# Kernel tuning notes

Hardware: AMD Instinct MI355X
Metric: run time of the kernel (lower is better)

## Reference

```python
import jax, jax.numpy as jnp
import numpy as np

N_NODES = 100000
N_EDGES = 3200000
F_IN = 256
N_CLASSES = 10


def setup_inputs() -> dict:
    key = jax.random.key(0)
    ks = jax.random.split(key, 10)
    x = jax.random.normal(ks[0], (N_NODES, F_IN), dtype=jnp.float32)
    edge_index = jax.random.randint(ks[1], (2, N_EDGES), 0, N_NODES, dtype=jnp.int64)
    def glorot(k, fan_in, fan_out):
        s = (6.0 / (fan_in + fan_out)) ** 0.5
        return jax.random.uniform(k, (fan_in, fan_out), jnp.float32, -s, s)
    return {
        "x": x,
        "edge_index": edge_index,
        "W_gcn": glorot(ks[2], F_IN, 64),
        "b_gcn": jnp.zeros((64,), jnp.float32),
        "W1": glorot(ks[3], 64, 32),
        "b1": jnp.zeros((32,), jnp.float32),
        "W2": glorot(ks[4], 32, 16),
        "b2": jnp.zeros((16,), jnp.float32),
        "W3": glorot(ks[5], 16, N_CLASSES),
        "b3": jnp.zeros((N_CLASSES,), jnp.float32),
    }


def gcn_conv(x, edge_index, W, b):
    # PyG GCNConv: x' = D^{-1/2} (A + I) D^{-1/2} (x W) + b, with self-loops.
    n = x.shape[0]
    loop = jnp.arange(n, dtype=edge_index.dtype)
    src = jnp.concatenate([edge_index[0], loop])  # [E+N]
    dst = jnp.concatenate([edge_index[1], loop])
    deg = jax.ops.segment_sum(jnp.ones(src.shape, jnp.float32), dst, num_segments=n)
    dinv = jnp.where(deg > 0, jax.lax.rsqrt(deg), 0.0)
    norm = dinv[src] * dinv[dst]  # [E+N]
    h = x @ W  # transform first (reduces message width to 64)
    msg = h[src] * norm[:, None]  # gather + scale
    out = jax.ops.segment_sum(msg, dst, num_segments=n)  # scatter-add
    return out + b


def reference(x, edge_index, W_gcn, b_gcn, W1, b1, W2, b2, W3, b3):
    # Dropout is a no-op in eval mode; reference uses deterministic eval math.
    h = jax.nn.relu(gcn_conv(x, edge_index, W_gcn, b_gcn))
    h = jax.nn.relu(h @ W1 + b1)
    h = jax.nn.relu(h @ W2 + b2)
    return h @ W3 + b3
```

## Files before the change

### kernel.cpp

```cpp
#include <hip/hip_runtime.h>

#define F_IN 256
#define CHUNK 8192

typedef short bf8_t __attribute__((ext_vector_type(8)));
typedef float f4_t  __attribute__((ext_vector_type(4)));

__device__ __forceinline__ unsigned short f2bf(float f) {
  unsigned u = __float_as_uint(f);
  unsigned r = (u + 0x7FFFu + ((u >> 16) & 1u)) >> 16;
  return (unsigned short)r;
}
#define BF_LO(d) __uint_as_float((d) << 16)
#define BF_HI(d) __uint_as_float((d) & 0xFFFF0000u)

__global__ __launch_bounds__(256) void gemm_mfma_kernel(
    const float* __restrict__ x, const float* __restrict__ W,
    const float* __restrict__ dinvp, unsigned short* __restrict__ hb, int M) {
  __shared__ short As[128][40];
  __shared__ short Bs[64][264];
  const int t = threadIdx.x;
  const int brow = blockIdx.x * 128;
  const int w = t >> 6;
  const int l = t & 63;
  const int mlane = l & 15;
  const int quad = l >> 4;

  for (int i = 0; i < 64; ++i) {
    const int flat = i * 256 + t;
    const int k = flat >> 6, n = flat & 63;
    Bs[n][k] = (short)f2bf(W[flat]);
  }

  f4_t acc[2][4];
#pragma unroll
  for (int a = 0; a < 2; ++a)
#pragma unroll
    for (int b = 0; b < 4; ++b) acc[a][b] = (f4_t){0.f, 0.f, 0.f, 0.f};

  for (int k0 = 0; k0 < F_IN; k0 += 32) {
    {
      const int q = t & 7;
      const int rbase = t >> 3;
#pragma unroll
      for (int j = 0; j < 4; ++j) {
        const int r = rbase + j * 32;
        const int row = brow + r;
        float4 v = make_float4(0.f, 0.f, 0.f, 0.f);
        if (row < M) v = *(const float4*)(x + (size_t)row * F_IN + k0 + (q << 2));
        short* p = &As[r][q << 2];
        p[0] = (short)f2bf(v.x);
        p[1] = (short)f2bf(v.y);
        p[2] = (short)f2bf(v.z);
        p[3] = (short)f2bf(v.w);
      }
    }
    __syncthreads();
    bf8_t afr[2], bfr[4];
#pragma unroll
    for (int mt = 0; mt < 2; ++mt)
      afr[mt] = *(const bf8_t*)&As[w * 32 + mt * 16 + mlane][quad << 3];
#pragma unroll
    for (int nt = 0; nt < 4; ++nt)
      bfr[nt] = *(const bf8_t*)&Bs[nt * 16 + mlane][k0 + (quad << 3)];
#pragma unroll
    for (int mt = 0; mt < 2; ++mt)
#pragma unroll
      for (int nt = 0; nt < 4; ++nt)
        acc[mt][nt] = __builtin_amdgcn_mfma_f32_16x16x32_bf16(
            afr[mt], bfr[nt], acc[mt][nt], 0, 0, 0);
    __syncthreads();
  }

#pragma unroll
  for (int mt = 0; mt < 2; ++mt) {
#pragma unroll
    for (int reg = 0; reg < 4; ++reg) {
      const int row = brow + w * 32 + mt * 16 + (quad << 2) + reg;
      if (row < M) {
        const float di = dinvp[row];
#pragma unroll
        for (int nt = 0; nt < 4; ++nt)
          hb[(size_t)row * 64 + nt * 16 + mlane] = f2bf(di * acc[mt][nt][reg]);
      }
    }
  }
}

__global__ __launch_bounds__(512) void sort_local_kernel(
    const int* __restrict__ src_arr, const int* __restrict__ dst_arr,
    int* __restrict__ espB, int* __restrict__ segStart, int* __restrict__ segCnt,
    int* __restrict__ bucketCount, int E, int NBK) {
  __shared__ int hist[512];
  __shared__ int s[512];
  __shared__ int cur[512];
  const int t = threadIdx.x;
  const int blk = blockIdx.x;
  const int base = blk * CHUNK;
  const int cnt = min(CHUNK, E - base);
  for (int i = t; i < NBK; i += 512) hist[i] = 0;
  __syncthreads();
  int pk[16], bk[16];
#pragma unroll
  for (int k = 0; k < 16; ++k) {
    const int i = t + k * 512;
    bk[k] = -1;
    if (i < cnt) {
      const int sv = src_arr[base + i];
      const int dv = dst_arr[base + i];
      pk[k] = sv | ((dv & 255) << 24);
      bk[k] = dv >> 8;
      atomicAdd(&hist[bk[k]], 1);
    }
  }
  __syncthreads();
  const int v = (t < NBK) ? hist[t] : 0;
  s[t] = v;
  __syncthreads();
#pragma unroll
  for (int off = 1; off < 512; off <<= 1) {
    int add = (t >= off) ? s[t - off] : 0;
    __syncthreads();
    s[t] += add;
    __syncthreads();
  }
  if (t < NBK) {
    const int excl = s[t] - v;
    cur[t] = excl;
    segStart[blk * NBK + t] = base + excl;
    segCnt[blk * NBK + t] = v;
    if (v) atomicAdd(&bucketCount[t], v);
  }
  __syncthreads();
#pragma unroll
  for (int k = 0; k < 16; ++k) {
    if (bk[k] >= 0) {
      const int pos = atomicAdd(&cur[bk[k]], 1);
      espB[base + pos] = pk[k];
    }
  }
}

__global__ __launch_bounds__(512) void scan_buckets_kernel(
    const int* __restrict__ bucketCount, int* __restrict__ bucketStart, int NBK) {
  __shared__ int s[512];
  const int t = threadIdx.x;
  const int v = (t < NBK) ? bucketCount[t] : 0;
  s[t] = v;
  __syncthreads();
#pragma unroll
  for (int off = 1; off < 512; off <<= 1) {
    int add = (t >= off) ? s[t - off] : 0;
    __syncthreads();
    s[t] += add;
    __syncthreads();
  }
  if (t < NBK) bucketStart[t] = s[t] - v;
  if (t == NBK - 1) bucketStart[NBK] = s[t];
}

__global__ __launch_bounds__(512) void fine_bin2_kernel(
    const int* __restrict__ espB, const int* __restrict__ segStart,
    const int* __restrict__ segCnt, const int* __restrict__ bucketStart,
    int* __restrict__ es, int* __restrict__ rowptr, float* __restrict__ dinvp,
    int N, int E, int NBK, int NCH) {
  __shared__ int segS[512];
  __shared__ int segC[512];
  __shared__ int sbuf[512];
  __shared__ int hist[256];
  __shared__ int cur[256];
  const int t = threadIdx.x;
  const int b = blockIdx.x;
  for (int i = t; i < 512; i += 512) { segS[i] = 0; segC[i] = 0; }
  if (t < 256) hist[t] = 0;
  __syncthreads();
  for (int i = t; i < NCH; i += 512) {
    segS[i] = segStart[i * NBK + b];
    segC[i] = segCnt[i * NBK + b];
  }
  __syncthreads();

  const int wid = t >> 6;
  const int lane = t & 63;

  for (int seg = wid; seg < NCH; seg += 8) {
    const int sS = segS[seg], c = segC[seg];
    for (int j = lane; j < c; j += 64)
      atomicAdd(&hist[((unsigned)espB[sS + j]) >> 24], 1);
  }
  __syncthreads();

  int v2 = 0;
  if (t < 256) { v2 = hist[t]; sbuf[t] = v2; }
  __syncthreads();
#pragma unroll
  for (int off = 1; off < 256; off <<= 1) {
    int add = 0;
    if (t < 256 && t >= off) add = sbuf[t - off];
    __syncthreads();
    if (t < 256) sbuf[t] += add;
    __syncthreads();
  }
  const int base = bucketStart[b];
  if (t < 256) {
    const int excl = sbuf[t] - v2;
    cur[t] = base + excl;
    const int node = b * 256 + t;
    if (node < N) {
      rowptr[node] = base + excl;
      dinvp[node] = rsqrtf((float)(v2 + 1));
    }
  }
  if (b == 0 && t == 0) rowptr[N] = E;
  __syncthreads();

  for (int seg = wid; seg < NCH; seg += 8) {
    const int sS = segS[seg], c = segC[seg];
    for (int j = lane; j < c; j += 64) {
      const int p = espB[sS + j];
      const int pos = atomicAdd(&cur[((unsigned)p) >> 24], 1);
      es[pos] = p & 0x00FFFFFF;
    }
  }
}

__global__ __launch_bounds__(256) void agg_csr_kernel(
    const unsigned short* __restrict__ hb, const int* __restrict__ es,
    const int* __restrict__ rowptr, const float* __restrict__ dinvp,
    float* __restrict__ agg, int N) {
  const int t = threadIdx.x;
  const int node = blockIdx.x * 4 + (t >> 6);
  if (node >= N) return;
  const int lane = t & 63;
  const int slot = lane >> 3;
  const int fq = (lane & 7) << 3;
  const int start = rowptr[node];
  const int end = rowptr[node + 1];

  float acc[8] = {0.f};
  int i = start + slot;
  for (; i + 8 < end; i += 16) {
    const int s0 = es[i];
    const int s1 = es[i + 8];
    const uint4 r0 = *(const uint4*)(hb + (size_t)s0 * 64 + fq);
    const uint4 r1 = *(const uint4*)(hb + (size_t)s1 * 64 + fq);
    acc[0] += BF_LO(r0.x) + BF_LO(r1.x);
    acc[1] += BF_HI(r0.x) + BF_HI(r1.x);
    acc[2] += BF_LO(r0.y) + BF_LO(r1.y);
    acc[3] += BF_HI(r0.y) + BF_HI(r1.y);
    acc[4] += BF_LO(r0.z) + BF_LO(r1.z);
    acc[5] += BF_HI(r0.z) + BF_HI(r1.z);
    acc[6] += BF_LO(r0.w) + BF_LO(r1.w);
    acc[7] += BF_HI(r0.w) + BF_HI(r1.w);
  }
  if (i < end) {
    const int s0 = es[i];
    const uint4 r0 = *(const uint4*)(hb + (size_t)s0 * 64 + fq);
    acc[0] += BF_LO(r0.x);
    acc[1] += BF_HI(r0.x);
    acc[2] += BF_LO(r0.y);
    acc[3] += BF_HI(r0.y);
    acc[4] += BF_LO(r0.z);
    acc[5] += BF_HI(r0.z);
    acc[6] += BF_LO(r0.w);
    acc[7] += BF_HI(r0.w);
  }
#pragma unroll
  for (int m = 8; m <= 32; m <<= 1)
#pragma unroll
    for (int j = 0; j < 8; ++j) acc[j] += __shfl_xor(acc[j], m, 64);

  if (slot == 0) {
    const float di = dinvp[node];
    float4 o0 = make_float4(acc[0] * di, acc[1] * di, acc[2] * di, acc[3] * di);
    float4 o1 = make_float4(acc[4] * di, acc[5] * di, acc[6] * di, acc[7] * di);
    float* ap = agg + (size_t)node * 64 + fq;
    *(float4*)(ap + 0) = o0;
    *(float4*)(ap + 4) = o1;
  }
}

__global__ __launch_bounds__(256) void mlp_mfma_kernel(
    const float* __restrict__ agg, const unsigned short* __restrict__ hb,
    const float* __restrict__ dinvp, const float* __restrict__ bg,
    const float* __restrict__ W1, const float* __restrict__ b1,
    const float* __restrict__ W2, const float* __restrict__ b2,
    const float* __restrict__ W3, const float* __restrict__ b3,
    float* __restrict__ out, int N) {
  __shared__ short g64[256 * 72];
  __shared__ short h2s[256 * 40];
  __shared__ short W1s[32 * 72];
  __shared__ short W2s[16 * 40];
  __shared__ short W3s[16 * 40];
  __shared__ float bgs[64], b1s[32], b2s[16], b3s[16];
  short* h1s = g64;

  const int t = threadIdx.x;
  const int node0 = blockIdx.x * 256;
  for (int i = t; i < 256 * 40; i += 256) h2s[i] = 0;
  for (int i = t; i < 16 * 40; i += 256) W3s[i] = 0;
  if (t < 64) bgs[t] = bg[t];
  if (t < 32) b1s[t] = b1[t];
  if (t < 16) { b2s[t] = b2[t]; b3s[t] = (t < 10) ? b3[t] : 0.f; }
  __syncthreads();
  for (int i = t; i < 2048; i += 256) { const int k = i >> 5, n = i & 31; W1s[n * 72 + k] = (short)f2bf(W1[i]); }
  for (int i = t; i < 512;  i += 256) { const int k = i >> 4, n = i & 15; W2s[n * 40 + k] = (short)f2bf(W2[i]); }
  if (t < 160) { const int k = t / 10, n = t % 10; W3s[n * 40 + k] = (short)f2bf(W3[t]); }
  {
    const int nd = min(node0 + t, N - 1);
    const float di = dinvp[nd];
    short* gr = &g64[t * 72];
    const float* ar = agg + (size_t)nd * 64;
    const unsigned short* hr = hb + (size_t)nd * 64;
#pragma unroll
    for (int k = 0; k < 64; k += 8) {
      const float4 a0 = *(const float4*)(ar + k);
      const float4 a1 = *(const float4*)(ar + k + 4);
      const uint4 r = *(const uint4*)(hr + k);
      gr[k + 0] = (short)f2bf(fmaxf(a0.x + di * BF_LO(r.x) + bgs[k + 0], 0.f));
      gr[k + 1] = (short)f2bf(fmaxf(a0.y + di * BF_HI(r.x) + bgs[k + 1], 0.f));
      gr[k + 2] = (short)f2bf(fmaxf(a0.z + di * BF_LO(r.y) + bgs[k + 2], 0.f));
      gr[k + 3] = (short)f2bf(fmaxf(a0.w + di * BF_HI(r.y) + bgs[k + 3], 0.f));
      gr[k + 4] = (short)f2bf(fmaxf(a1.x + di * BF_LO(r.z) + bgs[k + 4], 0.f));
      gr[k + 5] = (short)f2bf(fmaxf(a1.y + di * BF_HI(r.z) + bgs[k + 5], 0.f));
      gr[k + 6] = (short)f2bf(fmaxf(a1.z + di * BF_LO(r.w) + bgs[k + 6], 0.f));
      gr[k + 7] = (short)f2bf(fmaxf(a1.w + di * BF_HI(r.w) + bgs[k + 7], 0.f));
    }
  }
  __syncthreads();

  const int w = t >> 6;
  const int lane = t & 63;
  const int ml = lane & 15;
  const int quad = lane >> 4;

  bf8_t a1f[4][2], b1f[2][2];
#pragma unroll
  for (int mt = 0; mt < 4; ++mt)
#pragma unroll
    for (int ks = 0; ks < 2; ++ks)
      a1f[mt][ks] = *(const bf8_t*)&g64[(w * 64 + mt * 16 + ml) * 72 + ks * 32 + quad * 8];
#pragma unroll
  for (int nt = 0; nt < 2; ++nt)
#pragma unroll
    for (int ks = 0; ks < 2; ++ks)
      b1f[nt][ks] = *(const bf8_t*)&W1s[(nt * 16 + ml) * 72 + ks * 32 + quad * 8];
  f4_t acc1[4][2];
#pragma unroll
  for (int mt = 0; mt < 4; ++mt)
#pragma unroll
    for (int nt = 0; nt < 2; ++nt) acc1[mt][nt] = (f4_t){0.f, 0.f, 0.f, 0.f};
#pragma unroll
  for (int ks = 0; ks < 2; ++ks)
#pragma unroll
    for (int mt = 0; mt < 4; ++mt)
#pragma unroll
      for (int nt = 0; nt < 2; ++nt)
        acc1[mt][nt] = __builtin_amdgcn_mfma_f32_16x16x32_bf16(
            a1f[mt][ks], b1f[nt][ks], acc1[mt][nt], 0, 0, 0);
  __syncthreads();
#pragma unroll
  for (int mt = 0; mt < 4; ++mt)
#pragma unroll
    for (int nt = 0; nt < 2; ++nt)
#pragma unroll
      for (int reg = 0; reg < 4; ++reg) {
        const int row = w * 64 + mt * 16 + quad * 4 + reg;
        const int col = nt * 16 + ml;
        h1s[row * 40 + col] = (short)f2bf(fmaxf(acc1[mt][nt][reg] + b1s[col], 0.f));
      }
  __syncthreads();

  bf8_t a2f[4];
#pragma unroll
  for (int mt = 0; mt < 4; ++mt)
    a2f[mt] = *(const bf8_t*)&h1s[(w * 64 + mt * 16 + ml) * 40 + quad * 8];
  const bf8_t b2f = *(const bf8_t*)&W2s[ml * 40 + quad * 8];
  f4_t acc2[4];
#pragma unroll
  for (int mt = 0; mt < 4; ++mt) {
    acc2[mt] = (f4_t){0.f, 0.f, 0.f, 0.f};
    acc2[mt] = __builtin_amdgcn_mfma_f32_16x16x32_bf16(a2f[mt], b2f, acc2[mt], 0, 0, 0);
  }
  __syncthreads();
#pragma unroll
  for (int mt = 0; mt < 4; ++mt)
#pragma unroll
    for (int reg = 0; reg < 4; ++reg) {
      const int row = w * 64 + mt * 16 + quad * 4 + reg;
      h2s[row * 40 + ml] = (short)f2bf(fmaxf(acc2[mt][reg] + b2s[ml], 0.f));
    }
  __syncthreads();

  bf8_t a3f[4];
#pragma unroll
  for (int mt = 0; mt < 4; ++mt)
    a3f[mt] = *(const bf8_t*)&h2s[(w * 64 + mt * 16 + ml) * 40 + quad * 8];
  const bf8_t b3f = *(const bf8_t*)&W3s[ml * 40 + quad * 8];
#pragma unroll
  for (int mt = 0; mt < 4; ++mt) {
    f4_t acc3 = (f4_t){0.f, 0.f, 0.f, 0.f};
    acc3 = __builtin_amdgcn_mfma_f32_16x16x32_bf16(a3f[mt], b3f, acc3, 0, 0, 0);
#pragma unroll
    for (int reg = 0; reg < 4; ++reg) {
      const int node = node0 + w * 64 + mt * 16 + quad * 4 + reg;
      if (ml < 10 && node < N) out[(size_t)node * 10 + ml] = acc3[reg] + b3s[ml];
    }
  }
}

extern "C" void kernel_launch(void* const* d_in, const int* in_sizes, int n_in,
                              void* d_out, int out_size, void* d_ws, size_t ws_size,
                              hipStream_t stream) {
  const float* x     = (const float*)d_in[0];
  const int*   ei    = (const int*)d_in[1];
  const float* W_gcn = (const float*)d_in[2];
  const float* b_gcn = (const float*)d_in[3];
  const float* W1    = (const float*)d_in[4];
  const float* b1    = (const float*)d_in[5];
  const float* W2    = (const float*)d_in[6];
  const float* b2    = (const float*)d_in[7];
  const float* W3    = (const float*)d_in[8];
  const float* b3    = (const float*)d_in[9];
  float* out = (float*)d_out;

  const int N = in_sizes[0] / F_IN;
  const int E = in_sizes[1] / 2;
  const int* src = ei;
  const int* dst = ei + E;
  const int NBK = (N + 255) >> 8;
  const int NCH = (E + CHUNK - 1) / CHUNK;

  unsigned short* hb = (unsigned short*)d_ws;
  float* dinvp       = (float*)(hb + (size_t)N * 64);
  int*   es          = (int*)(dinvp + N);
  int*   rowptr      = es + E;
  int*   bucketCount = rowptr + N + 16;
  int*   bucketStart = bucketCount + 512;
  int*   espB        = bucketStart + 528;
  int*   segStart    = espB + E;
  int*   segCnt      = segStart + NCH * NBK;
  float* agg         = (float*)espB;

  hipMemsetAsync(bucketCount, 0, 512 * sizeof(int), stream);

  sort_local_kernel<<<NCH, 512, 0, stream>>>(
      src, dst, espB, segStart, segCnt, bucketCount, E, NBK);
  scan_buckets_kernel<<<1, 512, 0, stream>>>(bucketCount, bucketStart, NBK);
  fine_bin2_kernel<<<NBK, 512, 0, stream>>>(
      espB, segStart, segCnt, bucketStart, es, rowptr, dinvp, N, E, NBK, NCH);

  gemm_mfma_kernel<<<(N + 127) / 128, 256, 0, stream>>>(x, W_gcn, dinvp, hb, N);

  agg_csr_kernel<<<(N + 3) / 4, 256, 0, stream>>>(hb, es, rowptr, dinvp, agg, N);

  mlp_mfma_kernel<<<(N + 255) / 256, 256, 0, stream>>>(
      agg, hb, dinvp, b_gcn, W1, b1, W2, b2, W3, b3, out, N);
}
```

Measured before the change: 360.4 us.

## Load GEMM A fragments directly from global memory and pre-convert W to bf16

The GEMM now drops the LDS staging of x: each lane loads its own MFMA A fragment straight from global memory as two float4s and packs them to bf16, which removes the per-k-step __syncthreads barriers. A separate small kernel converts and transposes W_gcn to bf16 once, so each GEMM block copies B into LDS with vector loads instead of converting 16K floats itself. The trade-off is less coalesced global access for x (each lane reads 32 bytes per row), plus an extra kernel launch and a workspace buffer.

```diff
diff --git a/kernel.cpp b/kernel.cpp
--- a/kernel.cpp
+++ b/kernel.cpp
@@ -14,23 +14,43 @@
 #define BF_LO(d) __uint_as_float((d) << 16)
 #define BF_HI(d) __uint_as_float((d) & 0xFFFF0000u)
 
-__global__ __launch_bounds__(256) void gemm_mfma_kernel(
-    const float* __restrict__ x, const float* __restrict__ W,
+__device__ __forceinline__ bf8_t pack8(float4 a, float4 b) {
+  bf8_t r;
+  r[0] = (short)f2bf(a.x); r[1] = (short)f2bf(a.y);
+  r[2] = (short)f2bf(a.z); r[3] = (short)f2bf(a.w);
+  r[4] = (short)f2bf(b.x); r[5] = (short)f2bf(b.y);
+  r[6] = (short)f2bf(b.z); r[7] = (short)f2bf(b.w);
+  return r;
+}
+
+__global__ __launch_bounds__(256) void wprep_kernel(
+    const float* __restrict__ W, unsigned short* __restrict__ WbT) {
+  const int i = blockIdx.x * 256 + threadIdx.x;
+  const int k = i >> 6, n = i & 63;
+  WbT[n * 256 + k] = f2bf(W[i]);
+}
+
+__global__ __launch_bounds__(256) void gemm_direct_kernel(
+    const float* __restrict__ x, const unsigned short* __restrict__ WbT,
     const float* __restrict__ dinvp, unsigned short* __restrict__ hb, int M) {
-  __shared__ short As[128][40];
   __shared__ short Bs[64][264];
   const int t = threadIdx.x;
+  for (int i = t; i < 2048; i += 256) {
+    const int n = i >> 5, kq = (i & 31) << 3;
+    *(uint4*)&Bs[n][kq] = *(const uint4*)(WbT + n * 256 + kq);
+  }
+  __syncthreads();
+
   const int brow = blockIdx.x * 128;
   const int w = t >> 6;
   const int l = t & 63;
-  const int mlane = l & 15;
+  const int ml = l & 15;
   const int quad = l >> 4;
 
-  for (int i = 0; i < 64; ++i) {
-    const int flat = i * 256 + t;
-    const int k = flat >> 6, n = flat & 63;
-    Bs[n][k] = (short)f2bf(W[flat]);
-  }
+  const int r0 = min(brow + w * 32 + ml, M - 1);
+  const int r1 = min(brow + w * 32 + 16 + ml, M - 1);
+  const float* xr0 = x + (size_t)r0 * F_IN + (quad << 3);
+  const float* xr1 = x + (size_t)r1 * F_IN + (quad << 3);
 
   f4_t acc[2][4];
 #pragma unroll
@@ -38,38 +58,27 @@
 #pragma unroll
     for (int b = 0; b < 4; ++b) acc[a][b] = (f4_t){0.f, 0.f, 0.f, 0.f};
 
+#pragma unroll
   for (int k0 = 0; k0 < F_IN; k0 += 32) {
+    bf8_t afr[2];
     {
-      const int q = t & 7;
-      const int rbase = t >> 3;
-#pragma unroll
-      for (int j = 0; j < 4; ++j) {
-        const int r = rbase + j * 32;
-        const int row = brow + r;
-        float4 v = make_float4(0.f, 0.f, 0.f, 0.f);
-        if (row < M) v = *(const float4*)(x + (size_t)row * F_IN + k0 + (q << 2));
-        short* p = &As[r][q << 2];
-        p[0] = (short)f2bf(v.x);
-        p[1] = (short)f2bf(v.y);
-        p[2] = (short)f2bf(v.z);
-        p[3] = (short)f2bf(v.w);
-      }
-    }
-    __syncthreads();
-    bf8_t afr[2], bfr[4];
-#pragma unroll
-    for (int mt = 0; mt < 2; ++mt)
-      afr[mt] = *(const bf8_t*)&As[w * 32 + mt * 16 + mlane][quad << 3];
+      const float4 a0 = *(const float4*)(xr0 + k0);
+      const float4 a1 = *(const float4*)(xr0 + k0 + 4);
+      afr[0] = pack8(a0, a1);
+      const float4 c0 = *(const float4*)(xr1 + k0);
+      const float4 c1 = *(const float4*)(xr1 + k0 + 4);
+      afr[1] = pack8(c0, c1);
+    }
+    bf8_t bfr[4];
 #pragma unroll
     for (int nt = 0; nt < 4; ++nt)
-      bfr[nt] = *(const bf8_t*)&Bs[nt * 16 + mlane][k0 + (quad << 3)];
+      bfr[nt] = *(const bf8_t*)&Bs[nt * 16 + ml][k0 + (quad << 3)];
 #pragma unroll
     for (int mt = 0; mt < 2; ++mt)
 #pragma unroll
       for (int nt = 0; nt < 4; ++nt)
         acc[mt][nt] = __builtin_amdgcn_mfma_f32_16x16x32_bf16(
             afr[mt], bfr[nt], acc[mt][nt], 0, 0, 0);
-    __syncthreads();
   }
 
 #pragma unroll
@@ -81,7 +90,7 @@
         const float di = dinvp[row];
 #pragma unroll
         for (int nt = 0; nt < 4; ++nt)
-          hb[(size_t)row * 64 + nt * 16 + mlane] = f2bf(di * acc[mt][nt][reg]);
+          hb[(size_t)row * 64 + nt * 16 + ml] = f2bf(di * acc[mt][nt][reg]);
       }
     }
   }
@@ -440,17 +449,19 @@
   int*   espB        = bucketStart + 528;
   int*   segStart    = espB + E;
   int*   segCnt      = segStart + NCH * NBK;
+  unsigned short* WbT= (unsigned short*)(segCnt + NCH * NBK);
   float* agg         = (float*)espB;
 
   hipMemsetAsync(bucketCount, 0, 512 * sizeof(int), stream);
 
+  wprep_kernel<<<64, 256, 0, stream>>>(W_gcn, WbT);
   sort_local_kernel<<<NCH, 512, 0, stream>>>(
       src, dst, espB, segStart, segCnt, bucketCount, E, NBK);
   scan_buckets_kernel<<<1, 512, 0, stream>>>(bucketCount, bucketStart, NBK);
   fine_bin2_kernel<<<NBK, 512, 0, stream>>>(
       espB, segStart, segCnt, bucketStart, es, rowptr, dinvp, N, E, NBK, NCH);
 
-  gemm_mfma_kernel<<<(N + 127) / 128, 256, 0, stream>>>(x, W_gcn, dinvp, hb, N);
+  gemm_direct_kernel<<<(N + 127) / 128, 256, 0, stream>>>(x, WbT, dinvp, hb, N);
 
   agg_csr_kernel<<<(N + 3) / 4, 256, 0, stream>>>(hb, es, rowptr, dinvp, agg, N);
 
```

New measurement: 342.2 us. -5.0%, faster.
